# Kernel tuning notes

Measured on AMD Instinct MI355X. Metric: run time of the kernel, lower is better.

Reference implementation:

```python
import jax, jax.numpy as jnp
import numpy as np

B, C, H, W = 4, 64, 64, 64
Q = 192 * 192
IN_DIM = C * 9 + 2 + 2  # 580
HID = 256
OUT = 3
EPS_SHIFT = 1e-6
EPS_CLAMP = 1e-6


def setup_inputs() -> dict:
    key = jax.random.key(0)
    ks = jax.random.split(key, 10)
    feat = jax.random.normal(ks[0], (B, C, H, W), dtype=jnp.float32)
    coord = jax.random.uniform(ks[1], (B, Q, 2), dtype=jnp.float32, minval=-1.0, maxval=1.0)
    cell = jnp.full((B, Q, 2), 2.0 / 192.0, dtype=jnp.float32)
    def lin(k, fan_in, fan_out):
        return jax.random.normal(k, (fan_in, fan_out), dtype=jnp.float32) * (1.0 / np.sqrt(fan_in))
    return {
        "feat": feat, "coord": coord, "cell": cell,
        "w0": lin(ks[2], IN_DIM, HID), "b0": jnp.zeros((HID,), jnp.float32),
        "w1": lin(ks[3], HID, HID), "b1": jnp.zeros((HID,), jnp.float32),
        "w2": lin(ks[4], HID, HID), "b2": jnp.zeros((HID,), jnp.float32),
        "w3": lin(ks[5], HID, HID), "b3": jnp.zeros((HID,), jnp.float32),
        "w4": lin(ks[6], HID, OUT), "b4": jnp.zeros((OUT,), jnp.float32),
    }


def _mlp(x, w0, b0, w1, b1, w2, b2, w3, b3, w4, b4):
    h = jax.nn.relu(x @ w0 + b0)
    h = jax.nn.relu(h @ w1 + b1)
    h = jax.nn.relu(h @ w2 + b2)
    h = jax.nn.relu(h @ w3 + b3)
    return h @ w4 + b4


def _query_rgb(feat, coord, cell, params):
    b, c, h, w = feat.shape
    # F.unfold(feat, 3, padding=1): channel ordering c*9 + (kh*3 + kw)
    padded = jnp.pad(feat, ((0, 0), (0, 0), (1, 1), (1, 1)))
    shifts = jnp.stack([padded[:, :, kh:kh + h, kw:kw + w]
                        for kh in range(3) for kw in range(3)], axis=2)  # (B,C,9,H,W)
    feat_hw = shifts.reshape(b, c * 9, h, w).transpose(0, 2, 3, 1)  # (B,H,W,C9)

    rx = 1.0 / h  # 2 / H / 2
    ry = 1.0 / w
    bidx = jnp.arange(b)[:, None]
    cell_scaled = cell * jnp.array([h, w], dtype=cell.dtype)  # rel_cell

    preds, areas = [], []
    for vx in (-1.0, 1.0):
        for vy in (-1.0, 1.0):
            cx = jnp.clip(coord[:, :, 0] + vx * rx + EPS_SHIFT, -1 + EPS_CLAMP, 1 - EPS_CLAMP)
            cy = jnp.clip(coord[:, :, 1] + vy * ry + EPS_SHIFT, -1 + EPS_CLAMP, 1 - EPS_CLAMP)
            # grid_sample nearest, align_corners=False; grid is coord.flip(-1)
            # so cy indexes W (grid x) and cx indexes H (grid y)
            iy = jnp.clip(jnp.floor(((cx + 1) * h - 1) * 0.5 + 0.5), 0, h - 1).astype(jnp.int32)
            ix = jnp.clip(jnp.floor(((cy + 1) * w - 1) * 0.5 + 0.5), 0, w - 1).astype(jnp.int32)
            q_feat = feat_hw[bidx, iy, ix]  # (B,Q,C9)
            # feat_coord at (iy,ix): pixel-center coords in [-1,1]
            qcx = (iy.astype(coord.dtype) + 0.5) * (2.0 / h) - 1.0
            qcy = (ix.astype(coord.dtype) + 0.5) * (2.0 / w) - 1.0
            rel_x = (coord[:, :, 0] - qcx) * h
            rel_y = (coord[:, :, 1] - qcy) * w
            mid = jnp.concatenate(
                [q_feat, rel_x[..., None], rel_y[..., None], cell_scaled], axis=-1)
            preds.append(_mlp(mid, *params))  # (B,Q,3)
            areas.append(jnp.abs(rel_x * rel_y) + 1e-9)

    tot_area = areas[0] + areas[1] + areas[2] + areas[3]
    # local_ensemble swaps areas 0<->3 and 1<->2 before weighting
    order = (3, 2, 1, 0)
    result = sum(preds[i] * (areas[order[i]] / tot_area)[..., None] for i in range(4))
    return result


def reference(feat, coord, cell, w0, b0, w1, b1, w2, b2, w3, b3, w4, b4):
    params = (w0, b0, w1, b1, w2, b2, w3, b3, w4, b4)
    return _query_rgb(feat, coord, cell, params)
```

## Files before the change

### kernel.cpp

```cpp
#include <hip/hip_runtime.h>
#include <hip/hip_fp16.h>

typedef _Float16 f16;
typedef _Float16 f16x8 __attribute__((ext_vector_type(8)));
typedef _Float16 f16x4 __attribute__((ext_vector_type(4)));
typedef float f32x4 __attribute__((ext_vector_type(4)));

#define QQ 36864

__global__ void transpose_feat_k(const float* __restrict__ feat, f16* __restrict__ featT) {
    int idx = blockIdx.x * 256 + threadIdx.x;
    int c = idx & 63;
    int rest = idx >> 6;
    int x = rest & 63;
    int y = (rest >> 6) & 63;
    int b = rest >> 12;
    featT[idx] = (f16)feat[((b*64 + c)*64 + y)*64 + x];
}

__global__ void pack_w_k2(const float* __restrict__ w, const float* __restrict__ bias,
                          f16* __restrict__ dst, int nks, int nnt, int kreal,
                          int ncols, int perm) {
    int e = blockIdx.x * 256 + threadIdx.x;
    if (e >= nks * nnt * 512) return;
    int i    = e & 7;
    int lane = (e >> 3) & 63;
    int nt   = (e >> 9) % nnt;
    int ks   = (e >> 9) / nnt;
    int n = nt*16 + (lane & 15);
    int k = ks*32 + (lane >> 4)*8 + i;
    float v = 0.f;
    if (n < ncols) {
        if (k < kreal) {
            int rk = k;
            if (perm && k < 576) rk = (k & 63)*9 + (k >> 6);
            v = w[rk*ncols + n];
        } else if (k == kreal) {
            v = bias[n];
        }
    }
    dst[e] = (f16)v;
}

__global__ __launch_bounds__(256, 2)
void conv0_k(const f16* __restrict__ featT, const f16* __restrict__ pw0,
             float* __restrict__ P)
{
    __shared__ __align__(16) f16 Xs[2][64*64];

    const int t   = threadIdx.x;
    const int blk = blockIdx.x;
    const int by  = blk >> 6;
    const int y   = blk & 63;
    const int lane = t & 63;
    const int wv = t >> 6;
    const int l15 = lane & 15, g = lane >> 4;

    auto stage_ld = [&](int kc, int item) -> f16x8 {
        const int it = t + item*256;
        const int sr = it >> 3, sc = it & 7;
        const int kh = kc / 3, kw = kc - kh*3;
        const int yy = y + kh - 1;
        const int xx = sr + kw - 1;
        f16x8 v = {0,0,0,0,0,0,0,0};
        if (yy >= 0 && yy < 64 && xx >= 0 && xx < 64)
            v = *(const f16x8*)&featT[(((by*64 + yy)*64 + xx) << 6) + sc*8];
        return v;
    };
    auto stage_st = [&](int bufi, f16x8 v, int item) {
        const int it = t + item*256;
        const int sr = it >> 3, sc = it & 7;
        *(f16x8*)&Xs[bufi][sr*64 + ((sc ^ (sr & 7)) << 3)] = v;
    };
    auto ldXs = [&](int bufi, int j, int m) -> f16x8 {
        return *(const f16x8*)&Xs[bufi][m*64 + ((((j << 2) + g) ^ (m & 7)) << 3)];
    };
    auto ldB = [&](int ks, int nf) -> f16x8 {
        return *(const f16x8*)&pw0[((ks*16 + wv*4 + nf)*64 + lane)*8];
    };

    f32x4 acc[4][4];
    #pragma unroll
    for (int mf = 0; mf < 4; ++mf)
        #pragma unroll
        for (int nf = 0; nf < 4; ++nf)
            acc[mf][nf] = (f32x4){0.f, 0.f, 0.f, 0.f};

    f16x8 bc[4], bn[4];
    f16x8 s0a, s0b, s1a, s1b;
    s0a = stage_ld(0, 0); s0b = stage_ld(0, 1);
    #pragma unroll
    for (int nf = 0; nf < 4; ++nf) bc[nf] = ldB(0, nf);
    stage_st(0, s0a, 0); stage_st(0, s0b, 1);
    s1a = stage_ld(1, 0); s1b = stage_ld(1, 1);
    __syncthreads();

    #pragma unroll
    for (int kc = 0; kc < 9; ++kc) {
        #pragma unroll
        for (int j = 0; j < 2; ++j) {
            const int ks = kc*2 + j;
            #pragma unroll
            for (int nf = 0; nf < 4; ++nf) bn[nf] = ldB(ks + 1, nf);
            #pragma unroll
            for (int mf = 0; mf < 4; ++mf) {
                f16x8 a = ldXs(kc & 1, j, mf*16 + l15);
                #pragma unroll
                for (int nf = 0; nf < 4; ++nf)
                    acc[mf][nf] = __builtin_amdgcn_mfma_f32_16x16x32_f16(bc[nf], a, acc[mf][nf], 0, 0, 0);
            }
            #pragma unroll
            for (int nf = 0; nf < 4; ++nf) bc[nf] = bn[nf];
        }
        if (kc < 8) {
            if (kc & 1) { stage_st((kc + 1) & 1, s0a, 0); stage_st((kc + 1) & 1, s0b, 1); }
            else        { stage_st((kc + 1) & 1, s1a, 0); stage_st((kc + 1) & 1, s1b, 1); }
            if (kc < 7) {
                if (kc & 1) { s1a = stage_ld(kc + 2, 0); s1b = stage_ld(kc + 2, 1); }
                else        { s0a = stage_ld(kc + 2, 0); s0b = stage_ld(kc + 2, 1); }
            }
            __syncthreads();
        }
    }

    #pragma unroll
    for (int mf = 0; mf < 4; ++mf) {
        float* prow = &P[(blk*64 + mf*16 + l15)*256];
        #pragma unroll
        for (int nf = 0; nf < 4; ++nf)
            *(f32x4*)&prow[wv*64 + nf*16 + 4*g] = acc[mf][nf];
    }
}

__global__ __launch_bounds__(512, 4)
void liif_main_k(const float* __restrict__ P,
                 const f16* __restrict__ pw0, const f16* __restrict__ pw1,
                 const f16* __restrict__ pw2, const f16* __restrict__ pw3,
                 const f16* __restrict__ pw4,
                 const float* __restrict__ bias1, const float* __restrict__ bias2,
                 const float* __restrict__ bias3, const float* __restrict__ bias4,
                 const float* __restrict__ coord, const float* __restrict__ cell,
                 float* __restrict__ out)
{
    __shared__ __align__(16) f16 Hs[2][64*256];
    __shared__ int   pixs[64];
    __shared__ __align__(8) f16 tailA[64][4];
    __shared__ float areas[64];

    const int t   = threadIdx.x;
    const int blk = blockIdx.x;
    const int row0 = blk * 64;
    const int bb  = blk / 2304;

    if (t < 64) {
        const int r = t;
        const int grow = row0 + r;
        const int q = grow >> 2;
        const int s = grow & 3;
        const float c0  = coord[q*2 + 0];
        const float c1  = coord[q*2 + 1];
        const float ce0 = cell[q*2 + 0] * 64.f;
        const float ce1 = cell[q*2 + 1] * 64.f;
        const float vx = (s & 2) ? 1.f : -1.f;
        const float vy = (s & 1) ? 1.f : -1.f;
        float cx = c0 + vx*(1.f/64.f) + 1e-6f;
        cx = fminf(fmaxf(cx, -1.f + 1e-6f), 1.f - 1e-6f);
        float cy = c1 + vy*(1.f/64.f) + 1e-6f;
        cy = fminf(fmaxf(cy, -1.f + 1e-6f), 1.f - 1e-6f);
        float fiy = floorf(((cx + 1.f)*64.f - 1.f)*0.5f + 0.5f);
        fiy = fminf(fmaxf(fiy, 0.f), 63.f);
        float fix = floorf(((cy + 1.f)*64.f - 1.f)*0.5f + 0.5f);
        fix = fminf(fmaxf(fix, 0.f), 63.f);
        const float qcx = (fiy + 0.5f)*(2.f/64.f) - 1.f;
        const float qcy = (fix + 0.5f)*(2.f/64.f) - 1.f;
        const float rx = (c0 - qcx)*64.f;
        const float ry = (c1 - qcy)*64.f;
        pixs[r] = bb*4096 + (int)fiy*64 + (int)fix;
        tailA[r][0] = (f16)rx;  tailA[r][1] = (f16)ry;
        tailA[r][2] = (f16)ce0; tailA[r][3] = (f16)ce1;
        areas[r] = fabsf(rx*ry) + 1e-9f;
    }
    __syncthreads();

    const int lane = t & 63;
    const int wv = t >> 6;
    const int l15 = lane & 15, g = lane >> 4;

    auto ldHs = [&](const f16* hs, int ks, int m) -> f16x8 {
        return *(const f16x8*)&hs[m*256 + (((ks*4 + g) ^ (m & 7)) << 3)];
    };
    auto ldB = [&](const f16* __restrict__ pw, int ks, int nf) -> f16x8 {
        return *(const f16x8*)&pw[((ks*16 + wv*2 + nf)*64 + lane)*8];
    };

    f32x4 acc[4][2];
    f16x8 bc[2], bn[2];

    #pragma unroll
    for (int nf = 0; nf < 2; ++nf) bc[nf] = ldB(pw0, 18, nf);
    #pragma unroll
    for (int mf = 0; mf < 4; ++mf) {
        const float* prow = &P[pixs[mf*16 + l15]*256];
        #pragma unroll
        for (int nf = 0; nf < 2; ++nf)
            acc[mf][nf] = *(const f32x4*)&prow[wv*32 + nf*16 + 4*g];
    }
    #pragma unroll
    for (int mf = 0; mf < 4; ++mf) {
        f16x8 a = (f16x8){0,0,0,0,0,0,0,0};
        if (g == 0) {
            f16x4 tv = *(const f16x4*)&tailA[mf*16 + l15][0];
            a[0] = tv[0]; a[1] = tv[1]; a[2] = tv[2]; a[3] = tv[3];
            a[4] = (f16)1.f;
        }
        #pragma unroll
        for (int nf = 0; nf < 2; ++nf)
            acc[mf][nf] = __builtin_amdgcn_mfma_f32_16x16x32_f16(bc[nf], a, acc[mf][nf], 0, 0, 0);
    }
    #pragma unroll
    for (int nf = 0; nf < 2; ++nf) bc[nf] = ldB(pw1, 0, nf);

    auto writeback = [&](f16* hd, const float* __restrict__ bias) {
        #pragma unroll
        for (int nf = 0; nf < 2; ++nf) {
            const int nbase = wv*32 + nf*16 + 4*g;
            float bv0 = 0.f, bv1 = 0.f, bv2 = 0.f, bv3 = 0.f;
            if (bias) {
                bv0 = bias[nbase];     bv1 = bias[nbase + 1];
                bv2 = bias[nbase + 2]; bv3 = bias[nbase + 3];
            }
            #pragma unroll
            for (int mf = 0; mf < 4; ++mf) {
                const int m = mf*16 + l15;
                f16x4 pk;
                pk[0] = (f16)fmaxf(acc[mf][nf][0] + bv0, 0.f);
                pk[1] = (f16)fmaxf(acc[mf][nf][1] + bv1, 0.f);
                pk[2] = (f16)fmaxf(acc[mf][nf][2] + bv2, 0.f);
                pk[3] = (f16)fmaxf(acc[mf][nf][3] + bv3, 0.f);
                *(f16x4*)&hd[m*256 + (((nbase >> 3) ^ (m & 7)) << 3) + (nbase & 7)] = pk;
            }
        }
    };

    writeback(Hs[0], nullptr);
    __syncthreads();

    auto mlp_layer = [&](const f16* __restrict__ pw, const f16* __restrict__ pwn,
                         const float* __restrict__ bias, int src) {
        #pragma unroll
        for (int mf = 0; mf < 4; ++mf)
            #pragma unroll
            for (int nf = 0; nf < 2; ++nf)
                acc[mf][nf] = (f32x4){0.f, 0.f, 0.f, 0.f};
        #pragma unroll
        for (int ks = 0; ks < 8; ++ks) {
            #pragma unroll
            for (int nf = 0; nf < 2; ++nf)
                bn[nf] = (ks < 7) ? ldB(pw, ks + 1, nf) : ldB(pwn, 0, nf);
            #pragma unroll
            for (int mf = 0; mf < 4; ++mf) {
                f16x8 a = ldHs(Hs[src], ks, mf*16 + l15);
                #pragma unroll
                for (int nf = 0; nf < 2; ++nf)
                    acc[mf][nf] = __builtin_amdgcn_mfma_f32_16x16x32_f16(bc[nf], a, acc[mf][nf], 0, 0, 0);
            }
            #pragma unroll
            for (int nf = 0; nf < 2; ++nf) bc[nf] = bn[nf];
        }
        writeback(Hs[src ^ 1], bias);
        __syncthreads();
    };
    mlp_layer(pw1, pw2, bias1, 0);
    mlp_layer(pw2, pw3, bias2, 1);
    mlp_layer(pw3, pw3, bias3, 0);

    if (wv < 4) {
        const int m4 = wv * 16;
        f32x4 a4 = (f32x4){0.f, 0.f, 0.f, 0.f};
        #pragma unroll
        for (int ks = 0; ks < 8; ++ks) {
            f16x8 af = ldHs(Hs[1], ks, m4 + l15);
            f16x8 bf = *(const f16x8*)&pw4[(ks*64 + lane)*8];
            a4 = __builtin_amdgcn_mfma_f32_16x16x32_f16(af, bf, a4, 0, 0, 0);
        }
        if (l15 < 3) {
            const int base = m4 + 4*g;
            const float a0 = areas[base], a1 = areas[base+1];
            const float a2 = areas[base+2], a3 = areas[base+3];
            const float tot = a0 + a1 + a2 + a3;
            const float val = (a4[0]*a3 + a4[1]*a2 + a4[2]*a1 + a4[3]*a0) / tot
                              + bias4[l15];
            out[((row0 >> 2) + wv*4 + g)*3 + l15] = val;
        }
    }
}

extern "C" void kernel_launch(void* const* d_in, const int* in_sizes, int n_in,
                              void* d_out, int out_size, void* d_ws, size_t ws_size,
                              hipStream_t stream) {
    const float* feat  = (const float*)d_in[0];
    const float* coord = (const float*)d_in[1];
    const float* cell  = (const float*)d_in[2];
    const float* w0 = (const float*)d_in[3];
    const float* b0 = (const float*)d_in[4];
    const float* w1 = (const float*)d_in[5];
    const float* b1 = (const float*)d_in[6];
    const float* w2 = (const float*)d_in[7];
    const float* b2 = (const float*)d_in[8];
    const float* w3 = (const float*)d_in[9];
    const float* b3 = (const float*)d_in[10];
    const float* w4 = (const float*)d_in[11];
    const float* b4 = (const float*)d_in[12];
    float* out = (float*)d_out;

    f16* featT = (f16*)d_ws;
    f16* pw0 = featT + 4*64*64*64;
    f16* pw1 = pw0 + 19*16*512;
    f16* pw2 = pw1 + 8*16*512;
    f16* pw3 = pw2 + 8*16*512;
    f16* pw4 = pw3 + 8*16*512;
    float* P = (float*)(pw4 + 8*512);

    transpose_feat_k<<<4096, 256, 0, stream>>>(feat, featT);
    pack_w_k2<<<608, 256, 0, stream>>>(w0, b0, pw0, 19, 16, 580, 256, 1);
    pack_w_k2<<<256, 256, 0, stream>>>(w1, b1, pw1,  8, 16, 256, 256, 0);
    pack_w_k2<<<256, 256, 0, stream>>>(w2, b2, pw2,  8, 16, 256, 256, 0);
    pack_w_k2<<<256, 256, 0, stream>>>(w3, b3, pw3,  8, 16, 256, 256, 0);
    pack_w_k2<<< 16, 256, 0, stream>>>(w4, b4, pw4,  8,  1, 256,   3, 0);
    conv0_k<<<256, 256, 0, stream>>>(featT, pw0, P);
    liif_main_k<<<9216, 512, 0, stream>>>(P, pw0, pw1, pw2, pw3, pw4,
                                          b1, b2, b3, b4,
                                          coord, cell, out);
}
```

Before: 289.0 us.

## Switch hidden MLP layers to 32x32x16 MFMA with new weight packing

Replaces the 16x16x32 MFMA tiling of the hidden layers with 32x32x16 MFMA. Each wave now computes a 32-row by 64-column tile instead of 64 rows by 32 columns. Weights are repacked by a new pack kernel into the 32-wide fragment layout, and the activation loads from LDS are software-pipelined. The aim is fewer LDS reads per MFMA and better throughput per instruction, at the cost of different register use and a layout change that must stay consistent with the writeback swizzle.

```diff
diff --git a/kernel.cpp b/kernel.cpp
--- a/kernel.cpp
+++ b/kernel.cpp
@@ -5,6 +5,7 @@
 typedef _Float16 f16x8 __attribute__((ext_vector_type(8)));
 typedef _Float16 f16x4 __attribute__((ext_vector_type(4)));
 typedef float f32x4 __attribute__((ext_vector_type(4)));
+typedef float f32x16 __attribute__((ext_vector_type(16)));
 
 #define QQ 36864
 
@@ -42,6 +43,22 @@
     dst[e] = (f16)v;
 }
 
+__global__ void pack_w32_k(const float* __restrict__ w, const float* __restrict__ bias,
+                           f16* __restrict__ dst, int nks, int kreal) {
+    int e = blockIdx.x * 256 + threadIdx.x;
+    if (e >= nks * 8 * 512) return;
+    int i    = e & 7;
+    int lane = (e >> 3) & 63;
+    int nt   = (e >> 9) & 7;
+    int ks   = (e >> 9) >> 3;
+    int n = nt*32 + (lane & 31);
+    int k = ks*16 + (lane >> 5)*8 + i;
+    float v = 0.f;
+    if (k < kreal)      v = w[k*256 + n];
+    else if (k == kreal && bias) v = bias[n];
+    dst[e] = (f16)v;
+}
+
 __global__ __launch_bounds__(256, 2)
 void conv0_k(const f16* __restrict__ featT, const f16* __restrict__ pw0,
              float* __restrict__ P)
@@ -134,7 +151,7 @@
 
 __global__ __launch_bounds__(512, 4)
 void liif_main_k(const float* __restrict__ P,
-                 const f16* __restrict__ pw0, const f16* __restrict__ pw1,
+                 const f16* __restrict__ pw0t, const f16* __restrict__ pw1,
                  const f16* __restrict__ pw2, const f16* __restrict__ pw3,
                  const f16* __restrict__ pw4,
                  const float* __restrict__ bias1, const float* __restrict__ bias2,
@@ -184,62 +201,69 @@
 
     const int lane = t & 63;
     const int wv = t >> 6;
-    const int l15 = lane & 15, g = lane >> 4;
-
-    auto ldHs = [&](const f16* hs, int ks, int m) -> f16x8 {
-        return *(const f16x8*)&hs[m*256 + (((ks*4 + g) ^ (m & 7)) << 3)];
-    };
-    auto ldB = [&](const f16* __restrict__ pw, int ks, int nf) -> f16x8 {
-        return *(const f16x8*)&pw[((ks*16 + wv*2 + nf)*64 + lane)*8];
-    };
-
-    f32x4 acc[4][2];
-    f16x8 bc[2], bn[2];
-
-    #pragma unroll
-    for (int nf = 0; nf < 2; ++nf) bc[nf] = ldB(pw0, 18, nf);
-    #pragma unroll
-    for (int mf = 0; mf < 4; ++mf) {
-        const float* prow = &P[pixs[mf*16 + l15]*256];
-        #pragma unroll
-        for (int nf = 0; nf < 2; ++nf)
-            acc[mf][nf] = *(const f32x4*)&prow[wv*32 + nf*16 + 4*g];
-    }
-    #pragma unroll
-    for (int mf = 0; mf < 4; ++mf) {
-        f16x8 a = (f16x8){0,0,0,0,0,0,0,0};
-        if (g == 0) {
-            f16x4 tv = *(const f16x4*)&tailA[mf*16 + l15][0];
-            a[0] = tv[0]; a[1] = tv[1]; a[2] = tv[2]; a[3] = tv[3];
-            a[4] = (f16)1.f;
-        }
-        #pragma unroll
-        for (int nf = 0; nf < 2; ++nf)
-            acc[mf][nf] = __builtin_amdgcn_mfma_f32_16x16x32_f16(bc[nf], a, acc[mf][nf], 0, 0, 0);
-    }
-    #pragma unroll
-    for (int nf = 0; nf < 2; ++nf) bc[nf] = ldB(pw1, 0, nf);
+    const int l31 = lane & 31, h = lane >> 5;
+    const int mt  = wv & 1;
+    const int nt0 = (wv >> 1) * 2;
+    const int m32 = mt*32 + l31;
+
+    auto haddr = [&](int m, int c) -> int {
+        return m*256 + ((c ^ (m & 7)) << 3);
+    };
+    auto ldH32 = [&](const f16* hs, int ks) -> f16x8 {
+        return *(const f16x8*)&hs[haddr(m32, ks*2 + h)];
+    };
+    auto ldW32 = [&](const f16* __restrict__ pw, int ks, int j) -> f16x8 {
+        return *(const f16x8*)&pw[((ks*8 + nt0 + j)*64 + lane)*8];
+    };
+
+    f32x16 acc[2];
+    f16x8 wc[2], wn[2];
+
+    #pragma unroll
+    for (int j = 0; j < 2; ++j) wc[j] = ldW32(pw0t, 0, j);
+    {
+        const float* prow = &P[pixs[m32]*256];
+        #pragma unroll
+        for (int j = 0; j < 2; ++j)
+            #pragma unroll
+            for (int r2 = 0; r2 < 4; ++r2) {
+                f32x4 v = *(const f32x4*)&prow[(nt0 + j)*32 + 8*r2 + 4*h];
+                acc[j][r2*4+0] = v[0]; acc[j][r2*4+1] = v[1];
+                acc[j][r2*4+2] = v[2]; acc[j][r2*4+3] = v[3];
+            }
+    }
+    {
+        f16x8 tb = (f16x8){0,0,0,0,0,0,0,0};
+        if (h == 0) {
+            f16x4 tv = *(const f16x4*)&tailA[m32][0];
+            tb[0] = tv[0]; tb[1] = tv[1]; tb[2] = tv[2]; tb[3] = tv[3];
+            tb[4] = (f16)1.f;
+        }
+        #pragma unroll
+        for (int j = 0; j < 2; ++j)
+            acc[j] = __builtin_amdgcn_mfma_f32_32x32x16_f16(wc[j], tb, acc[j], 0, 0, 0);
+    }
+    #pragma unroll
+    for (int j = 0; j < 2; ++j) wc[j] = ldW32(pw1, 0, j);
 
     auto writeback = [&](f16* hd, const float* __restrict__ bias) {
         #pragma unroll
-        for (int nf = 0; nf < 2; ++nf) {
-            const int nbase = wv*32 + nf*16 + 4*g;
-            float bv0 = 0.f, bv1 = 0.f, bv2 = 0.f, bv3 = 0.f;
-            if (bias) {
-                bv0 = bias[nbase];     bv1 = bias[nbase + 1];
-                bv2 = bias[nbase + 2]; bv3 = bias[nbase + 3];
+        for (int j = 0; j < 2; ++j)
+            #pragma unroll
+            for (int r2 = 0; r2 < 4; ++r2) {
+                const int n0 = (nt0 + j)*32 + 8*r2 + 4*h;
+                float bv0 = 0.f, bv1 = 0.f, bv2 = 0.f, bv3 = 0.f;
+                if (bias) {
+                    bv0 = bias[n0];     bv1 = bias[n0 + 1];
+                    bv2 = bias[n0 + 2]; bv3 = bias[n0 + 3];
+                }
+                f16x4 pk;
+                pk[0] = (f16)fmaxf(acc[j][r2*4+0] + bv0, 0.f);
+                pk[1] = (f16)fmaxf(acc[j][r2*4+1] + bv1, 0.f);
+                pk[2] = (f16)fmaxf(acc[j][r2*4+2] + bv2, 0.f);
+                pk[3] = (f16)fmaxf(acc[j][r2*4+3] + bv3, 0.f);
+                *(f16x4*)&hd[haddr(m32, n0 >> 3) + (n0 & 7)] = pk;
             }
-            #pragma unroll
-            for (int mf = 0; mf < 4; ++mf) {
-                const int m = mf*16 + l15;
-                f16x4 pk;
-                pk[0] = (f16)fmaxf(acc[mf][nf][0] + bv0, 0.f);
-                pk[1] = (f16)fmaxf(acc[mf][nf][1] + bv1, 0.f);
-                pk[2] = (f16)fmaxf(acc[mf][nf][2] + bv2, 0.f);
-                pk[3] = (f16)fmaxf(acc[mf][nf][3] + bv3, 0.f);
-                *(f16x4*)&hd[m*256 + (((nbase >> 3) ^ (m & 7)) << 3) + (nbase & 7)] = pk;
-            }
-        }
     };
 
     writeback(Hs[0], nullptr);
@@ -248,24 +272,22 @@
     auto mlp_layer = [&](const f16* __restrict__ pw, const f16* __restrict__ pwn,
                          const float* __restrict__ bias, int src) {
         #pragma unroll
-        for (int mf = 0; mf < 4; ++mf)
-            #pragma unroll
-            for (int nf = 0; nf < 2; ++nf)
-                acc[mf][nf] = (f32x4){0.f, 0.f, 0.f, 0.f};
-        #pragma unroll
-        for (int ks = 0; ks < 8; ++ks) {
-            #pragma unroll
-            for (int nf = 0; nf < 2; ++nf)
-                bn[nf] = (ks < 7) ? ldB(pw, ks + 1, nf) : ldB(pwn, 0, nf);
-            #pragma unroll
-            for (int mf = 0; mf < 4; ++mf) {
-                f16x8 a = ldHs(Hs[src], ks, mf*16 + l15);
-                #pragma unroll
-                for (int nf = 0; nf < 2; ++nf)
-                    acc[mf][nf] = __builtin_amdgcn_mfma_f32_16x16x32_f16(bc[nf], a, acc[mf][nf], 0, 0, 0);
-            }
-            #pragma unroll
-            for (int nf = 0; nf < 2; ++nf) bc[nf] = bn[nf];
+        for (int j = 0; j < 2; ++j)
+            #pragma unroll
+            for (int e = 0; e < 16; ++e) acc[j][e] = 0.f;
+        f16x8 hc = ldH32(Hs[src], 0), hn;
+        #pragma unroll
+        for (int ks = 0; ks < 16; ++ks) {
+            #pragma unroll
+            for (int j = 0; j < 2; ++j)
+                wn[j] = (ks < 15) ? ldW32(pw, ks + 1, j) : ldW32(pwn, 0, j);
+            if (ks < 15) hn = ldH32(Hs[src], ks + 1);
+            #pragma unroll
+            for (int j = 0; j < 2; ++j)
+                acc[j] = __builtin_amdgcn_mfma_f32_32x32x16_f16(wc[j], hc, acc[j], 0, 0, 0);
+            #pragma unroll
+            for (int j = 0; j < 2; ++j) wc[j] = wn[j];
+            if (ks < 15) hc = hn;
         }
         writeback(Hs[src ^ 1], bias);
         __syncthreads();
@@ -275,11 +297,13 @@
     mlp_layer(pw3, pw3, bias3, 0);
 
     if (wv < 4) {
+        const int l15 = lane & 15, g = lane >> 4;
         const int m4 = wv * 16;
         f32x4 a4 = (f32x4){0.f, 0.f, 0.f, 0.f};
         #pragma unroll
         for (int ks = 0; ks < 8; ++ks) {
-            f16x8 af = ldHs(Hs[1], ks, m4 + l15);
+            const int m = m4 + l15;
+            f16x8 af = *(const f16x8*)&Hs[1][haddr(m, ks*4 + g)];
             f16x8 bf = *(const f16x8*)&pw4[(ks*64 + lane)*8];
             a4 = __builtin_amdgcn_mfma_f32_16x16x32_f16(af, bf, a4, 0, 0, 0);
         }
@@ -314,21 +338,23 @@
     float* out = (float*)d_out;
 
     f16* featT = (f16*)d_ws;
-    f16* pw0 = featT + 4*64*64*64;
-    f16* pw1 = pw0 + 19*16*512;
-    f16* pw2 = pw1 + 8*16*512;
-    f16* pw3 = pw2 + 8*16*512;
-    f16* pw4 = pw3 + 8*16*512;
-    float* P = (float*)(pw4 + 8*512);
+    f16* pw0  = featT + 4*64*64*64;
+    f16* pw4  = pw0 + 19*16*512;
+    f16* pw1  = pw4 + 8*512;
+    f16* pw2  = pw1 + 16*8*512;
+    f16* pw3  = pw2 + 16*8*512;
+    f16* pw0t = pw3 + 16*8*512;
+    float* P  = (float*)(pw0t + 8*512);
 
     transpose_feat_k<<<4096, 256, 0, stream>>>(feat, featT);
     pack_w_k2<<<608, 256, 0, stream>>>(w0, b0, pw0, 19, 16, 580, 256, 1);
-    pack_w_k2<<<256, 256, 0, stream>>>(w1, b1, pw1,  8, 16, 256, 256, 0);
-    pack_w_k2<<<256, 256, 0, stream>>>(w2, b2, pw2,  8, 16, 256, 256, 0);
-    pack_w_k2<<<256, 256, 0, stream>>>(w3, b3, pw3,  8, 16, 256, 256, 0);
     pack_w_k2<<< 16, 256, 0, stream>>>(w4, b4, pw4,  8,  1, 256,   3, 0);
+    pack_w32_k<<<256, 256, 0, stream>>>(w1, nullptr, pw1, 16, 256);
+    pack_w32_k<<<256, 256, 0, stream>>>(w2, nullptr, pw2, 16, 256);
+    pack_w32_k<<<256, 256, 0, stream>>>(w3, nullptr, pw3, 16, 256);
+    pack_w32_k<<< 16, 256, 0, stream>>>(w0 + 576*256, b0, pw0t, 1, 4);
     conv0_k<<<256, 256, 0, stream>>>(featT, pw0, P);
-    liif_main_k<<<9216, 512, 0, stream>>>(P, pw0, pw1, pw2, pw3, pw4,
+    liif_main_k<<<9216, 512, 0, stream>>>(P, pw0t, pw1, pw2, pw3, pw4,
                                           b1, b2, b3, b4,
                                           coord, cell, out);
 }
```

Result: slower. 384.5 us (+33.1%).
